# Kernel tuning notes

Hardware: AMD Instinct MI355X
Metric: run time of the kernel (lower is better)

Reference implementation:

```python
import jax, jax.numpy as jnp
import numpy as np

B, S, D, E = 16, 2048, 1024, 1024
NEG = -1e13  # not_mask_sign from the original module


def setup_inputs() -> dict:
    key = jax.random.key(0)
    k1, k2, k3, k4, k5, k6 = jax.random.split(key, 6)
    return {
        "Q": jax.random.normal(k1, (B, S, D), dtype=jnp.float32),
        "K": jax.random.normal(k2, (B, S, D), dtype=jnp.float32),
        "V": jax.random.normal(k3, (B, S, D), dtype=jnp.float32),
        "pad_idxs": jax.random.randint(k4, (B,), 0, S, dtype=jnp.int64),
        "W": jax.random.normal(k5, (D, E), dtype=jnp.float32) * (1.0 / np.sqrt(D)),
        "b": jax.random.normal(k6, (E,), dtype=jnp.float32) * 0.01,
    }


def reference(Q, K, V, pad_idxs, W, b):
    d = Q.shape[2]
    # [B, S, S] attention scores
    scores = jnp.einsum("bqd,bkd->bqk", Q, K) / jnp.sqrt(jnp.asarray(d, Q.dtype))
    # Faithful to original: mask entries where row>=pad AND col>=pad
    idx = jnp.arange(scores.shape[1])
    p = pad_idxs[:, None, None]
    mask = (idx[None, :, None] >= p) & (idx[None, None, :] >= p)  # [B,S,S]
    scores = jnp.where(mask, jnp.asarray(NEG, scores.dtype), scores)
    attn = jax.nn.softmax(scores, axis=2)
    out = jnp.einsum("bqk,bkd->bqd", attn, V)
    return out @ W + b
```

## Files before the change

kernel.cpp:

```cpp
#include <hip/hip_runtime.h>

typedef unsigned short u16;
typedef unsigned int u32;
typedef long long ll;
typedef __attribute__((ext_vector_type(8))) short bf16x8;
typedef __attribute__((ext_vector_type(8))) unsigned short u16x8;
typedef __attribute__((ext_vector_type(4))) float f32x4;

__device__ __forceinline__ u16 f2bf(float f) {
  u32 x = __float_as_uint(f);
  x += 0x7fffu + ((x >> 16) & 1u);
  return (u16)(x >> 16);
}
__device__ __forceinline__ float bf2f(u16 u) {
  return __uint_as_float(((u32)u) << 16);
}

__device__ __forceinline__ int read_pad(const int* pw, int z) {
  int odd = pw[1] | pw[3] | pw[5] | pw[7] | pw[9] | pw[11] | pw[13] | pw[15];
  return (odd == 0) ? pw[2 * z] : pw[z];
}

__device__ __forceinline__ void stage_unit(const u16* gsrc, int gld, u16* dst,
                                           int ks, int wid, int lane) {
  const int rsub = lane >> 2;
  const int gk = ks * 32 + (((lane & 3) ^ ((lane >> 3) & 3)) * 8);
#pragma unroll
  for (int q = 0; q < 2; ++q) {
    const int r0 = (q * 8 + wid) * 16;
    __builtin_amdgcn_global_load_lds(
        (const __attribute__((address_space(1))) void*)(gsrc + (ll)(r0 + rsub) * gld + gk),
        (__attribute__((address_space(3))) void*)(dst + r0 * 32),
        16, 0, 0);
  }
}

template<int EPI>
__global__ __launch_bounds__(512, 2) void gemm8(
    const u16* __restrict__ A, const u16* __restrict__ B, void* __restrict__ C,
    int Kdim, int lda, int ldb, int ldc, ll sA, ll sB, ll sC,
    const int* __restrict__ pad, const float* __restrict__ bias,
    int NX, int NXY, int nwg) {
  __shared__ __align__(16) u16 ldsA[2][2 * 8192];
  __shared__ __align__(16) u16 ldsB[2][2 * 8192];

  const int orig = blockIdx.x;
  const int q8 = nwg >> 3, r8 = nwg & 7;
  const int xcd = orig & 7, inner = orig >> 3;
  const int wg = (xcd < r8 ? xcd * (q8 + 1) : r8 * (q8 + 1) + (xcd - r8) * q8) + inner;
  const int z = wg / NXY;
  const int rem = wg - z * NXY;
  const int by = rem / NX;
  const int bx = rem - by * NX;

  const int tid = threadIdx.x;
  const int wid = tid >> 6, lane = tid & 63;
  const int lr = lane & 15, lg = lane >> 4;
  const int wr = wid >> 2;
  const int wn64 = (wid & 3) * 64;
  const int bm = by * 256, bn = bx * 256;
  const u16* Ab = A + (ll)z * sA + (ll)bm * lda;
  const u16* Bb = B + (ll)z * sB + (ll)bn * ldb;

  const int aoff = lr * 32 + ((lg ^ ((lr >> 1) & 3)) * 8);

  f32x4 acc[8][4];
#pragma unroll
  for (int i = 0; i < 8; ++i)
#pragma unroll
    for (int j = 0; j < 4; ++j) acc[i][j] = (f32x4)0.0f;

#pragma unroll
  for (int p = 0; p < 4; ++p) {
    const int ks = p >> 1;
    if (p & 1) stage_unit(Bb, ldb, &ldsB[0][ks * 8192], ks, wid, lane);
    else       stage_unit(Ab, lda, &ldsA[0][ks * 8192], ks, wid, lane);
  }
  asm volatile("s_waitcnt vmcnt(4)" ::: "memory");
  __builtin_amdgcn_s_barrier();

  const int NT = Kdim >> 6;
  for (int t = 0; t < NT; ++t) {
    const int c = t & 1;
    u16* A_cur = &ldsA[c][0];
    u16* B_cur = &ldsB[c][0];
    u16* A_nxt = &ldsA[c ^ 1][0];
    u16* B_nxt = &ldsB[c ^ 1][0];
    const u16* Agn = Ab + (t + 1) * 64;
    const u16* Bgn = Bb + (t + 1) * 64;
    const bool stage = (t + 1 < NT);
    const bool last = (t + 1 == NT);
#pragma unroll
    for (int ks = 0; ks < 2; ++ks) {
      bf16x8 av[4], bv[4];
#pragma unroll
      for (int i = 0; i < 4; ++i) {
        bv[i] = *(const bf16x8*)(B_cur + ks * 8192 + (wn64 + i * 16) * 32 + aoff);
        av[i] = *(const bf16x8*)(A_cur + ks * 8192 + (wr * 128 + i * 16) * 32 + aoff);
      }
      if (stage) stage_unit(Agn, lda, A_nxt + ks * 8192, ks, wid, lane);
      __builtin_amdgcn_s_barrier();
      __builtin_amdgcn_s_setprio(1);
#pragma unroll
      for (int i = 0; i < 4; ++i)
#pragma unroll
        for (int j = 0; j < 4; ++j)
          acc[i][j] = __builtin_amdgcn_mfma_f32_16x16x32_bf16(
              av[i], bv[j], acc[i][j], 0, 0, 0);
      __builtin_amdgcn_s_setprio(0);
      __builtin_amdgcn_s_barrier();
#pragma unroll
      for (int i = 0; i < 4; ++i)
        av[i] = *(const bf16x8*)(A_cur + ks * 8192 +
                                 (wr * 128 + (4 + i) * 16) * 32 + aoff);
      if (stage) stage_unit(Bgn, ldb, B_nxt + ks * 8192, ks, wid, lane);
      __builtin_amdgcn_s_barrier();
      __builtin_amdgcn_s_setprio(1);
#pragma unroll
      for (int i = 0; i < 4; ++i)
#pragma unroll
        for (int j = 0; j < 4; ++j)
          acc[4 + i][j] = __builtin_amdgcn_mfma_f32_16x16x32_bf16(
              av[i], bv[j], acc[4 + i][j], 0, 0, 0);
      __builtin_amdgcn_s_setprio(0);
      if (ks == 0) {
        if (last) asm volatile("s_waitcnt vmcnt(0)" ::: "memory");
        else      asm volatile("s_waitcnt vmcnt(4)" ::: "memory");
      } else if (!last) {
        asm volatile("s_waitcnt vmcnt(4)" ::: "memory");
      }
      __builtin_amdgcn_s_barrier();
    }
  }

  int p = 0;
  if constexpr (EPI == 0) p = read_pad(pad, z);
#pragma unroll
  for (int mf = 0; mf < 8; ++mf) {
    const int rowb = bm + wr * 128 + mf * 16 + 4 * lg;
#pragma unroll
    for (int nf = 0; nf < 4; ++nf) {
      const int col = bn + wn64 + nf * 16 + lr;
#pragma unroll
      for (int rg = 0; rg < 4; ++rg) {
        const int r = rowb + rg;
        if constexpr (EPI == 0) {
          float v = acc[mf][nf][rg] * 0.03125f;
          if (r >= p && col >= p) v = -1e13f;
          ((u16*)C)[(ll)z * sC + (ll)r * ldc + col] = f2bf(v);
        } else if constexpr (EPI == 1) {
          ((u16*)C)[(ll)z * sC + (ll)r * ldc + col] = f2bf(acc[mf][nf][rg]);
        } else {
          ((float*)C)[(ll)z * sC + (ll)r * ldc + col] = acc[mf][nf][rg] + bias[col];
        }
      }
    }
  }
}

__global__ __launch_bounds__(256) void cvt_bf16(const float* __restrict__ src,
                                                u16* __restrict__ dst) {
  const ll i = ((ll)blockIdx.x * 256 + threadIdx.x) * 8;
  const float4 a = *(const float4*)(src + i);
  const float4 b = *(const float4*)(src + i + 4);
  u16x8 v;
  v[0] = f2bf(a.x); v[1] = f2bf(a.y); v[2] = f2bf(a.z); v[3] = f2bf(a.w);
  v[4] = f2bf(b.x); v[5] = f2bf(b.y); v[6] = f2bf(b.z); v[7] = f2bf(b.w);
  *(u16x8*)(dst + i) = v;
}

__global__ __launch_bounds__(256) void transpose_cvt(
    const float* __restrict__ src, u16* __restrict__ dst, int R, int C,
    ll sS, ll sD) {
  __shared__ u16 t[64][65];
  const int tid = threadIdx.x;
  const int r0 = blockIdx.y * 64, c0 = blockIdx.x * 64;
  const float* s = src + (ll)blockIdx.z * sS;
  u16* d = dst + (ll)blockIdx.z * sD;
#pragma unroll
  for (int it = 0; it < 16; ++it) {
    const int idx = it * 256 + tid;
    const int r = idx >> 6, c = idx & 63;
    t[r][c] = f2bf(s[(ll)(r0 + r) * C + c0 + c]);
  }
  __syncthreads();
#pragma unroll
  for (int it = 0; it < 16; ++it) {
    const int idx = it * 256 + tid;
    const int rr = idx >> 6, cc = idx & 63;
    d[(ll)(c0 + rr) * R + r0 + cc] = t[cc][rr];
  }
}

template<bool MASKED>
__global__ __launch_bounds__(256) void softmax_rows(u16* __restrict__ P,
                                                    const int* __restrict__ pad) {
  const int wid = threadIdx.x >> 6, lane = threadIdx.x & 63;
  const ll row = (ll)blockIdx.x * 4 + wid;
  const int z = (int)(row >> 11);
  const int r = (int)(row & 2047);
  int p = 0;
  bool rmask = false;
  if constexpr (MASKED) {
    p = read_pad(pad, z);
    rmask = (r >= p);
  }
  u16* ptr = P + row * 2048;
  float s[32];
#pragma unroll
  for (int i = 0; i < 4; ++i) {
    const u16x8 v = *(const u16x8*)(ptr + i * 512 + lane * 8);
#pragma unroll
    for (int j = 0; j < 8; ++j) {
      float x = bf2f(v[j]);
      if constexpr (MASKED) {
        const int col = i * 512 + lane * 8 + j;
        x *= 0.03125f;
        if (rmask && col >= p) x = -1e13f;
      }
      s[i * 8 + j] = x;
    }
  }
  float m = s[0];
#pragma unroll
  for (int i = 1; i < 32; ++i) m = fmaxf(m, s[i]);
#pragma unroll
  for (int o = 1; o < 64; o <<= 1) m = fmaxf(m, __shfl_xor(m, o));
  float sum = 0.0f;
#pragma unroll
  for (int i = 0; i < 32; ++i) {
    s[i] = __expf(s[i] - m);
    sum += s[i];
  }
#pragma unroll
  for (int o = 1; o < 64; o <<= 1) sum += __shfl_xor(sum, o);
  const float inv = 1.0f / sum;
#pragma unroll
  for (int i = 0; i < 4; ++i) {
    u16x8 v;
#pragma unroll
    for (int j = 0; j < 8; ++j) v[j] = f2bf(s[i * 8 + j] * inv);
    *(u16x8*)(ptr + i * 512 + lane * 8) = v;
  }
}

__device__ __forceinline__ void stage_f32(const float* src, ll base, int ld,
                                          u16* lds, int tid) {
#pragma unroll
  for (int p = 0; p < 4; ++p) {
    int chunk = p * 256 + tid;
    int r = chunk >> 3, slot = chunk & 7;
    const float* s = src + base + (ll)r * ld + slot * 8;
    const float4 a = *(const float4*)s;
    const float4 b = *(const float4*)(s + 4);
    u16x8 v;
    v[0] = f2bf(a.x); v[1] = f2bf(a.y); v[2] = f2bf(a.z); v[3] = f2bf(a.w);
    v[4] = f2bf(b.x); v[5] = f2bf(b.y); v[6] = f2bf(b.z); v[7] = f2bf(b.w);
    *(u16x8*)(lds + r * 64 + (slot ^ (r & 7)) * 8) = v;
  }
}

__global__ __launch_bounds__(256) void gemm_f32in(
    const float* __restrict__ A, const float* __restrict__ B,
    u16* __restrict__ C, int Kdim, int lda, int ldb, int ldc,
    ll sA, ll sB, ll sC) {
  __shared__ __align__(16) u16 As[128 * 64];
  __shared__ __align__(16) u16 Bs[128 * 64];
  const int tid = threadIdx.x;
  const int z = blockIdx.z;
  const int bm = blockIdx.y * 128, bn = blockIdx.x * 128;
  const ll abase = (ll)z * sA + (ll)bm * lda;
  const ll bbase = (ll)z * sB + (ll)bn * ldb;
  const int wid = tid >> 6, lane = tid & 63;
  const int wm = (wid >> 1) * 64, wn = (wid & 1) * 64;
  const int lr = lane & 15, lg = lane >> 4;

  f32x4 acc[4][4];
#pragma unroll
  for (int i = 0; i < 4; ++i)
#pragma unroll
    for (int j = 0; j < 4; ++j) acc[i][j] = (f32x4)0.0f;

  for (int k0 = 0; k0 < Kdim; k0 += 64) {
    __syncthreads();
    stage_f32(A, abase + k0, lda, As, tid);
    stage_f32(B, bbase + k0, ldb, Bs, tid);
    __syncthreads();
#pragma unroll
    for (int kk = 0; kk < 2; ++kk) {
      bf16x8 av[4], bv[4];
#pragma unroll
      for (int i = 0; i < 4; ++i) {
        const int ra = wm + i * 16 + lr;
        av[i] = *(const bf16x8*)(As + ra * 64 + (((kk * 4 + lg) ^ (ra & 7)) * 8));
        const int rb = wn + i * 16 + lr;
        bv[i] = *(const bf16x8*)(Bs + rb * 64 + (((kk * 4 + lg) ^ (rb & 7)) * 8));
      }
#pragma unroll
      for (int i = 0; i < 4; ++i)
#pragma unroll
        for (int j = 0; j < 4; ++j)
          acc[i][j] = __builtin_amdgcn_mfma_f32_16x16x32_bf16(av[i], bv[j],
                                                              acc[i][j], 0, 0, 0);
    }
  }
#pragma unroll
  for (int i = 0; i < 4; ++i) {
    const int rowb = bm + wm + i * 16 + 4 * lg;
#pragma unroll
    for (int j = 0; j < 4; ++j) {
      const int col = bn + wn + j * 16 + lr;
#pragma unroll
      for (int rg = 0; rg < 4; ++rg)
        C[(ll)z * sC + (ll)(rowb + rg) * ldc + col] = f2bf(acc[i][j][rg]);
    }
  }
}

extern "C" void kernel_launch(void* const* d_in, const int* in_sizes, int n_in,
                              void* d_out, int out_size, void* d_ws,
                              size_t ws_size, hipStream_t stream) {
  const float* Q = (const float*)d_in[0];
  const float* Km = (const float*)d_in[1];
  const float* V = (const float*)d_in[2];
  const int* pad = (const int*)d_in[3];
  const float* W = (const float*)d_in[4];
  const float* bias = (const float*)d_in[5];
  float* out = (float*)d_out;

  const int B = 16, S = 2048, D = 1024, E = 1024;
  const ll SS = (ll)S * S, SD = (ll)S * D;

  u16* P = (u16*)d_out;
  char* ws = (char*)d_ws;

  const size_t MB64 = (size_t)B * S * D * 2;
  const size_t szWt = (size_t)D * E * 2;

  if (ws_size >= 3 * MB64 + szWt) {
    u16* Qb = (u16*)ws;
    u16* Kb = (u16*)(ws + MB64);
    u16* Vt = (u16*)(ws + 2 * MB64);
    u16* Wt = (u16*)(ws + 3 * MB64);
    u16* X = Qb;

    const int nv = (int)(((ll)B * S * D) / (8 * 256));
    cvt_bf16<<<nv, 256, 0, stream>>>(Q, Qb);
    cvt_bf16<<<nv, 256, 0, stream>>>(Km, Kb);
    transpose_cvt<<<dim3(D / 64, S / 64, B), 256, 0, stream>>>(V, Vt, S, D, SD, SD);
    transpose_cvt<<<dim3(E / 64, D / 64, 1), 256, 0, stream>>>(W, Wt, D, E, 0, 0);

    gemm8<0><<<dim3(1024), 512, 0, stream>>>(
        Qb, Kb, P, D, D, D, S, SD, SD, SS, pad, nullptr, 8, 64, 1024);
    softmax_rows<false><<<dim3(B * S / 4), 256, 0, stream>>>(P, pad);
    gemm8<1><<<dim3(512), 512, 0, stream>>>(
        P, Vt, X, S, S, S, D, SS, SD, SD, nullptr, nullptr, 4, 32, 512);
    gemm8<2><<<dim3(512), 512, 0, stream>>>(
        X, Wt, out, D, D, D, E, 0, 0, 0, nullptr, bias, 4, 512, 512);
  } else if (ws_size >= 2 * MB64 + szWt) {
    u16* Vt = (u16*)ws;
    u16* Wt = (u16*)(ws + MB64);
    u16* X = (u16*)(ws + MB64 + szWt);

    transpose_cvt<<<dim3(D / 64, S / 64, B), 256, 0, stream>>>(V, Vt, S, D, SD, SD);
    transpose_cvt<<<dim3(E / 64, D / 64, 1), 256, 0, stream>>>(W, Wt, D, E, 0, 0);
    gemm_f32in<<<dim3(S / 128, S / 128, B), 256, 0, stream>>>(
        Q, Km, P, D, D, D, S, SD, SD, SS);
    softmax_rows<true><<<dim3(B * S / 4), 256, 0, stream>>>(P, pad);
    gemm8<1><<<dim3(512), 512, 0, stream>>>(
        P, Vt, X, S, S, S, D, SS, SD, SD, nullptr, nullptr, 4, 32, 512);
    gemm8<2><<<dim3(512), 512, 0, stream>>>(
        X, Wt, out, D, D, D, E, 0, 0, 0, nullptr, bias, 4, 512, 512);
  } else {
    u16* Wt = (u16*)ws;
    u16* Vtb = (u16*)(ws + szWt);
    u16* X = (u16*)(ws + szWt + (size_t)D * S * 2);

    transpose_cvt<<<dim3(E / 64, D / 64, 1), 256, 0, stream>>>(W, Wt, D, E, 0, 0);
    gemm_f32in<<<dim3(S / 128, S / 128, B), 256, 0, stream>>>(
        Q, Km, P, D, D, D, S, SD, SD, SS);
    softmax_rows<true><<<dim3(B * S / 4), 256, 0, stream>>>(P, pad);
    for (int b = 0; b < B; ++b) {
      transpose_cvt<<<dim3(D / 64, S / 64, 1), 256, 0, stream>>>(
          V + (ll)b * SD, Vtb, S, D, 0, 0);
      gemm8<1><<<dim3(32), 512, 0, stream>>>(
          P + (ll)b * SS, Vtb, X + (ll)b * SD, S, S, S, D, 0, 0, 0, nullptr,
          nullptr, 4, 32, 32);
    }
    gemm8<2><<<dim3(512), 512, 0, stream>>>(
        X, Wt, out, D, D, D, E, 0, 0, 0, nullptr, bias, 4, 512, 512);
  }
}
```

Measured before the change: 525.8 us.

## Issue both A and B prefetches up front and halve barriers per k-step

```diff
diff --git a/kernel.cpp b/kernel.cpp
--- a/kernel.cpp
+++ b/kernel.cpp
@@ -88,17 +88,22 @@
     u16* B_nxt = &ldsB[c ^ 1][0];
     const u16* Agn = Ab + (t + 1) * 64;
     const u16* Bgn = Bb + (t + 1) * 64;
-    const bool stage = (t + 1 < NT);
-    const bool last = (t + 1 == NT);
+    const bool stg = (t + 1 < NT);
 #pragma unroll
     for (int ks = 0; ks < 2; ++ks) {
-      bf16x8 av[4], bv[4];
+      if (stg) {
+        stage_unit(Agn, lda, A_nxt + ks * 8192, ks, wid, lane);
+        stage_unit(Bgn, ldb, B_nxt + ks * 8192, ks, wid, lane);
+      }
+      bf16x8 bv[4], a0[4], a1[4];
 #pragma unroll
       for (int i = 0; i < 4; ++i) {
         bv[i] = *(const bf16x8*)(B_cur + ks * 8192 + (wn64 + i * 16) * 32 + aoff);
-        av[i] = *(const bf16x8*)(A_cur + ks * 8192 + (wr * 128 + i * 16) * 32 + aoff);
-      }
-      if (stage) stage_unit(Agn, lda, A_nxt + ks * 8192, ks, wid, lane);
+        a0[i] = *(const bf16x8*)(A_cur + ks * 8192 + (wr * 128 + i * 16) * 32 + aoff);
+        a1[i] = *(const bf16x8*)(A_cur + ks * 8192 + (wr * 128 + (4 + i) * 16) * 32 + aoff);
+      }
+      if (stg)            asm volatile("s_waitcnt vmcnt(4)" ::: "memory");
+      else if (ks == 0)   asm volatile("s_waitcnt vmcnt(0)" ::: "memory");
       __builtin_amdgcn_s_barrier();
       __builtin_amdgcn_s_setprio(1);
 #pragma unroll
@@ -106,30 +111,14 @@
 #pragma unroll
         for (int j = 0; j < 4; ++j)
           acc[i][j] = __builtin_amdgcn_mfma_f32_16x16x32_bf16(
-              av[i], bv[j], acc[i][j], 0, 0, 0);
-      __builtin_amdgcn_s_setprio(0);
-      __builtin_amdgcn_s_barrier();
-#pragma unroll
-      for (int i = 0; i < 4; ++i)
-        av[i] = *(const bf16x8*)(A_cur + ks * 8192 +
-                                 (wr * 128 + (4 + i) * 16) * 32 + aoff);
-      if (stage) stage_unit(Bgn, ldb, B_nxt + ks * 8192, ks, wid, lane);
-      __builtin_amdgcn_s_barrier();
-      __builtin_amdgcn_s_setprio(1);
+              a0[i], bv[j], acc[i][j], 0, 0, 0);
 #pragma unroll
       for (int i = 0; i < 4; ++i)
 #pragma unroll
         for (int j = 0; j < 4; ++j)
           acc[4 + i][j] = __builtin_amdgcn_mfma_f32_16x16x32_bf16(
-              av[i], bv[j], acc[4 + i][j], 0, 0, 0);
+              a1[i], bv[j], acc[4 + i][j], 0, 0, 0);
       __builtin_amdgcn_s_setprio(0);
-      if (ks == 0) {
-        if (last) asm volatile("s_waitcnt vmcnt(0)" ::: "memory");
-        else      asm volatile("s_waitcnt vmcnt(4)" ::: "memory");
-      } else if (!last) {
-        asm volatile("s_waitcnt vmcnt(4)" ::: "memory");
-      }
-      __builtin_amdgcn_s_barrier();
     }
   }
 
```

Result: slower. 626.8 us (+19.2%).

## Deepen GEMM K-loop prefetch to stage half-tiles one step further ahead

Applied to the files above, without the earlier changes.

```diff
diff --git a/kernel.cpp b/kernel.cpp
--- a/kernel.cpp
+++ b/kernel.cpp
@@ -70,67 +70,97 @@
 #pragma unroll
     for (int j = 0; j < 4; ++j) acc[i][j] = (f32x4)0.0f;
 
-#pragma unroll
-  for (int p = 0; p < 4; ++p) {
-    const int ks = p >> 1;
-    if (p & 1) stage_unit(Bb, ldb, &ldsB[0][ks * 8192], ks, wid, lane);
-    else       stage_unit(Ab, lda, &ldsA[0][ks * 8192], ks, wid, lane);
-  }
-  asm volatile("s_waitcnt vmcnt(4)" ::: "memory");
+  const int NT = Kdim >> 6;
+
+  stage_unit(Ab, lda, &ldsA[0][0], 0, wid, lane);
+  stage_unit(Bb, ldb, &ldsB[0][0], 0, wid, lane);
+  stage_unit(Ab, lda, &ldsA[0][8192], 1, wid, lane);
+  stage_unit(Bb, ldb, &ldsB[0][8192], 1, wid, lane);
+  if (NT > 1) {
+    stage_unit(Ab + 64, lda, &ldsA[1][0], 0, wid, lane);
+    stage_unit(Bb + 64, ldb, &ldsB[1][0], 0, wid, lane);
+  }
+  asm volatile("s_waitcnt vmcnt(8)" ::: "memory");
   __builtin_amdgcn_s_barrier();
 
-  const int NT = Kdim >> 6;
   for (int t = 0; t < NT; ++t) {
     const int c = t & 1;
-    u16* A_cur = &ldsA[c][0];
-    u16* B_cur = &ldsB[c][0];
-    u16* A_nxt = &ldsA[c ^ 1][0];
-    u16* B_nxt = &ldsB[c ^ 1][0];
-    const u16* Agn = Ab + (t + 1) * 64;
-    const u16* Bgn = Bb + (t + 1) * 64;
-    const bool stage = (t + 1 < NT);
-    const bool last = (t + 1 == NT);
-#pragma unroll
-    for (int ks = 0; ks < 2; ++ks) {
-      bf16x8 av[4], bv[4];
-#pragma unroll
-      for (int i = 0; i < 4; ++i) {
-        bv[i] = *(const bf16x8*)(B_cur + ks * 8192 + (wn64 + i * 16) * 32 + aoff);
-        av[i] = *(const bf16x8*)(A_cur + ks * 8192 + (wr * 128 + i * 16) * 32 + aoff);
-      }
-      if (stage) stage_unit(Agn, lda, A_nxt + ks * 8192, ks, wid, lane);
-      __builtin_amdgcn_s_barrier();
-      __builtin_amdgcn_s_setprio(1);
-#pragma unroll
-      for (int i = 0; i < 4; ++i)
-#pragma unroll
-        for (int j = 0; j < 4; ++j)
-          acc[i][j] = __builtin_amdgcn_mfma_f32_16x16x32_bf16(
-              av[i], bv[j], acc[i][j], 0, 0, 0);
-      __builtin_amdgcn_s_setprio(0);
-      __builtin_amdgcn_s_barrier();
-#pragma unroll
-      for (int i = 0; i < 4; ++i)
-        av[i] = *(const bf16x8*)(A_cur + ks * 8192 +
-                                 (wr * 128 + (4 + i) * 16) * 32 + aoff);
-      if (stage) stage_unit(Bgn, ldb, B_nxt + ks * 8192, ks, wid, lane);
-      __builtin_amdgcn_s_barrier();
-      __builtin_amdgcn_s_setprio(1);
-#pragma unroll
-      for (int i = 0; i < 4; ++i)
-#pragma unroll
-        for (int j = 0; j < 4; ++j)
-          acc[4 + i][j] = __builtin_amdgcn_mfma_f32_16x16x32_bf16(
-              av[i], bv[j], acc[4 + i][j], 0, 0, 0);
-      __builtin_amdgcn_s_setprio(0);
-      if (ks == 0) {
-        if (last) asm volatile("s_waitcnt vmcnt(0)" ::: "memory");
-        else      asm volatile("s_waitcnt vmcnt(4)" ::: "memory");
-      } else if (!last) {
-        asm volatile("s_waitcnt vmcnt(4)" ::: "memory");
-      }
-      __builtin_amdgcn_s_barrier();
-    }
+    u16* Ac = &ldsA[c][0];
+    u16* Bc = &ldsB[c][0];
+    const bool s1 = (t + 1 < NT), s2 = (t + 2 < NT);
+    const u16* Ag1 = Ab + (t + 1) * 64;
+    const u16* Bg1 = Bb + (t + 1) * 64;
+    const u16* Ag2 = Ab + (t + 2) * 64;
+    const u16* Bg2 = Bb + (t + 2) * 64;
+    bf16x8 bv[4], av[4];
+
+#pragma unroll
+    for (int i = 0; i < 4; ++i) {
+      bv[i] = *(const bf16x8*)(Bc + (wn64 + i * 16) * 32 + aoff);
+      av[i] = *(const bf16x8*)(Ac + (wr * 128 + i * 16) * 32 + aoff);
+    }
+    if (s1) stage_unit(Ag1, lda, &ldsA[c ^ 1][8192], 1, wid, lane);
+    __builtin_amdgcn_s_barrier();
+    __builtin_amdgcn_s_setprio(1);
+#pragma unroll
+    for (int i = 0; i < 4; ++i)
+#pragma unroll
+      for (int j = 0; j < 4; ++j)
+        acc[i][j] = __builtin_amdgcn_mfma_f32_16x16x32_bf16(av[i], bv[j],
+                                                            acc[i][j], 0, 0, 0);
+    __builtin_amdgcn_s_setprio(0);
+    __builtin_amdgcn_s_barrier();
+
+#pragma unroll
+    for (int i = 0; i < 4; ++i)
+      av[i] = *(const bf16x8*)(Ac + (wr * 128 + (4 + i) * 16) * 32 + aoff);
+    if (s1) stage_unit(Bg1, ldb, &ldsB[c ^ 1][8192], 1, wid, lane);
+    __builtin_amdgcn_s_barrier();
+    __builtin_amdgcn_s_setprio(1);
+#pragma unroll
+    for (int i = 0; i < 4; ++i)
+#pragma unroll
+      for (int j = 0; j < 4; ++j)
+        acc[4 + i][j] = __builtin_amdgcn_mfma_f32_16x16x32_bf16(
+            av[i], bv[j], acc[4 + i][j], 0, 0, 0);
+    __builtin_amdgcn_s_setprio(0);
+    if (s1) asm volatile("s_waitcnt vmcnt(8)" ::: "memory");
+    else    asm volatile("s_waitcnt vmcnt(0)" ::: "memory");
+    __builtin_amdgcn_s_barrier();
+
+#pragma unroll
+    for (int i = 0; i < 4; ++i) {
+      bv[i] = *(const bf16x8*)(Bc + 8192 + (wn64 + i * 16) * 32 + aoff);
+      av[i] = *(const bf16x8*)(Ac + 8192 + (wr * 128 + i * 16) * 32 + aoff);
+    }
+    if (s2) stage_unit(Ag2, lda, &ldsA[c][0], 0, wid, lane);
+    __builtin_amdgcn_s_barrier();
+    __builtin_amdgcn_s_setprio(1);
+#pragma unroll
+    for (int i = 0; i < 4; ++i)
+#pragma unroll
+      for (int j = 0; j < 4; ++j)
+        acc[i][j] = __builtin_amdgcn_mfma_f32_16x16x32_bf16(av[i], bv[j],
+                                                            acc[i][j], 0, 0, 0);
+    __builtin_amdgcn_s_setprio(0);
+    __builtin_amdgcn_s_barrier();
+
+#pragma unroll
+    for (int i = 0; i < 4; ++i)
+      av[i] = *(const bf16x8*)(Ac + 8192 + (wr * 128 + (4 + i) * 16) * 32 + aoff);
+    if (s2) stage_unit(Bg2, ldb, &ldsB[c][0], 0, wid, lane);
+    __builtin_amdgcn_s_barrier();
+    __builtin_amdgcn_s_setprio(1);
+#pragma unroll
+    for (int i = 0; i < 4; ++i)
+#pragma unroll
+      for (int j = 0; j < 4; ++j)
+        acc[4 + i][j] = __builtin_amdgcn_mfma_f32_16x16x32_bf16(
+            av[i], bv[j], acc[4 + i][j], 0, 0, 0);
+    __builtin_amdgcn_s_setprio(0);
+    if (s2)      asm volatile("s_waitcnt vmcnt(8)" ::: "memory");
+    else if (s1) asm volatile("s_waitcnt vmcnt(4)" ::: "memory");
+    __builtin_amdgcn_s_barrier();
   }
 
   int p = 0;
```

After: 556.7 us. 5.9% more time.

## Fuse softmax exp into QK GEMM epilogue and defer normalization to PV GEMM

Applied to the files above, without the earlier changes.

```diff
diff --git a/kernel.cpp b/kernel.cpp
--- a/kernel.cpp
+++ b/kernel.cpp
@@ -40,7 +40,7 @@
     const u16* __restrict__ A, const u16* __restrict__ B, void* __restrict__ C,
     int Kdim, int lda, int ldb, int ldc, ll sA, ll sB, ll sC,
     const int* __restrict__ pad, const float* __restrict__ bias,
-    int NX, int NXY, int nwg) {
+    float* __restrict__ lsum, int NX, int NXY, int nwg) {
   __shared__ __align__(16) u16 ldsA[2][2 * 8192];
   __shared__ __align__(16) u16 ldsB[2][2 * 8192];
 
@@ -137,25 +137,51 @@
   if constexpr (EPI == 0) p = read_pad(pad, z);
 #pragma unroll
   for (int mf = 0; mf < 8; ++mf) {
-    const int rowb = bm + wr * 128 + mf * 16 + 4 * lg;
-#pragma unroll
-    for (int nf = 0; nf < 4; ++nf) {
-      const int col = bn + wn64 + nf * 16 + lr;
-#pragma unroll
-      for (int rg = 0; rg < 4; ++rg) {
-        const int r = rowb + rg;
-        if constexpr (EPI == 0) {
-          float v = acc[mf][nf][rg] * 0.03125f;
-          if (r >= p && col >= p) v = -1e13f;
-          ((u16*)C)[(ll)z * sC + (ll)r * ldc + col] = f2bf(v);
-        } else if constexpr (EPI == 1) {
-          ((u16*)C)[(ll)z * sC + (ll)r * ldc + col] = f2bf(acc[mf][nf][rg]);
-        } else {
-          ((float*)C)[(ll)z * sC + (ll)r * ldc + col] = acc[mf][nf][rg] + bias[col];
+#pragma unroll
+    for (int rg = 0; rg < 4; ++rg) {
+      const int row = bm + wr * 128 + mf * 16 + 4 * lg + rg;
+      if constexpr (EPI == 0) {
+        float part = 0.0f;
+#pragma unroll
+        for (int nf = 0; nf < 4; ++nf) {
+          const int col = bn + wn64 + nf * 16 + lr;
+          float e;
+          if (row >= p && col >= p) e = (p == 0) ? 1.0f : 0.0f;
+          else e = __expf(acc[mf][nf][rg] * 0.03125f);
+          part += e;
+          ((u16*)C)[(ll)z * sC + (ll)row * ldc + col] = f2bf(e);
+        }
+        part += __shfl_xor(part, 1);
+        part += __shfl_xor(part, 2);
+        part += __shfl_xor(part, 4);
+        part += __shfl_xor(part, 8);
+        if (lr == 0) atomicAdd(&lsum[z * 2048 + row], part);
+      } else if constexpr (EPI == 3) {
+        const float linv = 1.0f / lsum[z * 2048 + row];
+#pragma unroll
+        for (int nf = 0; nf < 4; ++nf) {
+          const int col = bn + wn64 + nf * 16 + lr;
+          ((u16*)C)[(ll)z * sC + (ll)row * ldc + col] =
+              f2bf(acc[mf][nf][rg] * linv);
+        }
+      } else {
+#pragma unroll
+        for (int nf = 0; nf < 4; ++nf) {
+          const int col = bn + wn64 + nf * 16 + lr;
+          if constexpr (EPI == 1) {
+            ((u16*)C)[(ll)z * sC + (ll)row * ldc + col] = f2bf(acc[mf][nf][rg]);
+          } else {
+            ((float*)C)[(ll)z * sC + (ll)row * ldc + col] =
+                acc[mf][nf][rg] + bias[col];
+          }
         }
       }
     }
   }
+}
+
+__global__ __launch_bounds__(256) void zerof(float* __restrict__ p) {
+  p[blockIdx.x * 256 + threadIdx.x] = 0.0f;
 }
 
 __global__ __launch_bounds__(256) void cvt_bf16(const float* __restrict__ src,
@@ -192,19 +218,14 @@
   }
 }
 
-template<bool MASKED>
 __global__ __launch_bounds__(256) void softmax_rows(u16* __restrict__ P,
                                                     const int* __restrict__ pad) {
   const int wid = threadIdx.x >> 6, lane = threadIdx.x & 63;
   const ll row = (ll)blockIdx.x * 4 + wid;
   const int z = (int)(row >> 11);
   const int r = (int)(row & 2047);
-  int p = 0;
-  bool rmask = false;
-  if constexpr (MASKED) {
-    p = read_pad(pad, z);
-    rmask = (r >= p);
-  }
+  const int p = read_pad(pad, z);
+  const bool rmask = (r >= p);
   u16* ptr = P + row * 2048;
   float s[32];
 #pragma unroll
@@ -212,12 +233,9 @@
     const u16x8 v = *(const u16x8*)(ptr + i * 512 + lane * 8);
 #pragma unroll
     for (int j = 0; j < 8; ++j) {
-      float x = bf2f(v[j]);
-      if constexpr (MASKED) {
-        const int col = i * 512 + lane * 8 + j;
-        x *= 0.03125f;
-        if (rmask && col >= p) x = -1e13f;
-      }
+      const int col = i * 512 + lane * 8 + j;
+      float x = bf2f(v[j]) * 0.03125f;
+      if (rmask && col >= p) x = -1e13f;
       s[i * 8 + j] = x;
     }
   }
@@ -336,27 +354,29 @@
 
   const size_t MB64 = (size_t)B * S * D * 2;
   const size_t szWt = (size_t)D * E * 2;
-
-  if (ws_size >= 3 * MB64 + szWt) {
+  const size_t szL = (size_t)B * S * 4;
+
+  if (ws_size >= 3 * MB64 + szWt + szL) {
     u16* Qb = (u16*)ws;
     u16* Kb = (u16*)(ws + MB64);
     u16* Vt = (u16*)(ws + 2 * MB64);
     u16* Wt = (u16*)(ws + 3 * MB64);
+    float* lsum = (float*)(ws + 3 * MB64 + szWt);
     u16* X = Qb;
 
     const int nv = (int)(((ll)B * S * D) / (8 * 256));
+    zerof<<<dim3(B * S / 256), 256, 0, stream>>>(lsum);
     cvt_bf16<<<nv, 256, 0, stream>>>(Q, Qb);
     cvt_bf16<<<nv, 256, 0, stream>>>(Km, Kb);
     transpose_cvt<<<dim3(D / 64, S / 64, B), 256, 0, stream>>>(V, Vt, S, D, SD, SD);
     transpose_cvt<<<dim3(E / 64, D / 64, 1), 256, 0, stream>>>(W, Wt, D, E, 0, 0);
 
     gemm8<0><<<dim3(1024), 512, 0, stream>>>(
-        Qb, Kb, P, D, D, D, S, SD, SD, SS, pad, nullptr, 8, 64, 1024);
-    softmax_rows<false><<<dim3(B * S / 4), 256, 0, stream>>>(P, pad);
-    gemm8<1><<<dim3(512), 512, 0, stream>>>(
-        P, Vt, X, S, S, S, D, SS, SD, SD, nullptr, nullptr, 4, 32, 512);
+        Qb, Kb, P, D, D, D, S, SD, SD, SS, pad, nullptr, lsum, 8, 64, 1024);
+    gemm8<3><<<dim3(512), 512, 0, stream>>>(
+        P, Vt, X, S, S, S, D, SS, SD, SD, nullptr, nullptr, lsum, 4, 32, 512);
     gemm8<2><<<dim3(512), 512, 0, stream>>>(
-        X, Wt, out, D, D, D, E, 0, 0, 0, nullptr, bias, 4, 512, 512);
+        X, Wt, out, D, D, D, E, 0, 0, 0, nullptr, bias, nullptr, 4, 512, 512);
   } else if (ws_size >= 2 * MB64 + szWt) {
     u16* Vt = (u16*)ws;
     u16* Wt = (u16*)(ws + MB64);
@@ -366,11 +386,11 @@
     transpose_cvt<<<dim3(E / 64, D / 64, 1), 256, 0, stream>>>(W, Wt, D, E, 0, 0);
     gemm_f32in<<<dim3(S / 128, S / 128, B), 256, 0, stream>>>(
         Q, Km, P, D, D, D, S, SD, SD, SS);
-    softmax_rows<true><<<dim3(B * S / 4), 256, 0, stream>>>(P, pad);
+    softmax_rows<<<dim3(B * S / 4), 256, 0, stream>>>(P, pad);
     gemm8<1><<<dim3(512), 512, 0, stream>>>(
-        P, Vt, X, S, S, S, D, SS, SD, SD, nullptr, nullptr, 4, 32, 512);
+        P, Vt, X, S, S, S, D, SS, SD, SD, nullptr, nullptr, nullptr, 4, 32, 512);
     gemm8<2><<<dim3(512), 512, 0, stream>>>(
-        X, Wt, out, D, D, D, E, 0, 0, 0, nullptr, bias, 4, 512, 512);
+        X, Wt, out, D, D, D, E, 0, 0, 0, nullptr, bias, nullptr, 4, 512, 512);
   } else {
     u16* Wt = (u16*)ws;
     u16* Vtb = (u16*)(ws + szWt);
@@ -379,15 +399,15 @@
     transpose_cvt<<<dim3(E / 64, D / 64, 1), 256, 0, stream>>>(W, Wt, D, E, 0, 0);
     gemm_f32in<<<dim3(S / 128, S / 128, B), 256, 0, stream>>>(
         Q, Km, P, D, D, D, S, SD, SD, SS);
-    softmax_rows<true><<<dim3(B * S / 4), 256, 0, stream>>>(P, pad);
+    softmax_rows<<<dim3(B * S / 4), 256, 0, stream>>>(P, pad);
     for (int b = 0; b < B; ++b) {
       transpose_cvt<<<dim3(D / 64, S / 64, 1), 256, 0, stream>>>(
           V + (ll)b * SD, Vtb, S, D, 0, 0);
       gemm8<1><<<dim3(32), 512, 0, stream>>>(
           P + (ll)b * SS, Vtb, X + (ll)b * SD, S, S, S, D, 0, 0, 0, nullptr,
-          nullptr, 4, 32, 32);
+          nullptr, nullptr, 4, 32, 32);
     }
     gemm8<2><<<dim3(512), 512, 0, stream>>>(
-        X, Wt, out, D, D, D, E, 0, 0, 0, nullptr, bias, 4, 512, 512);
-  }
-}
+        X, Wt, out, D, D, D, E, 0, 0, 0, nullptr, bias, nullptr, 4, 512, 512);
+  }
+}
```

New measurement: 541.0 us. +2.9%, slower.
